# Kernel optimization log

Measured on AMD Instinct MI355X. Metric: run time of the kernel, lower is better.

## Reference

```python
import jax, jax.numpy as jnp
import numpy as np

B, N, H, NH, P = 32, 400, 512, 8, 3
DK = H // NH
SCALE = DK ** -0.5
EPS = 1e-5


def _ln(x, g, b):
    m = jnp.mean(x, axis=-1, keepdims=True)
    v = jnp.mean((x - m) ** 2, axis=-1, keepdims=True)
    return (x - m) * jax.lax.rsqrt(v + EPS) * g + b


def _split(x):  # [B,N,H] -> [B,h,N,dk]
    return x.reshape(x.shape[0], x.shape[1], NH, DK).transpose(0, 2, 1, 3)


def _merge(x):  # [B,h,N,dk] -> [B,N,H]
    return x.transpose(0, 2, 1, 3).reshape(x.shape[0], x.shape[2], H)


def _attn(q, k, v, mask):
    s = jnp.einsum('bhid,bhjd->bhij', q, k) * SCALE
    s = s * (1.0 + mask[:, None])  # learned multiplicative prior mask
    p = jax.nn.softmax(s, axis=-1)
    return jnp.einsum('bhij,bhjd->bhid', p, v)


def _weight_gen(pri, z, C, wq, keys, wf, bf):
    # pooled token query attends over the num_priors prior matrices
    qv = jnp.mean(z @ wq, axis=1)  # [B,H]
    aw = jax.nn.softmax((qv @ keys.T) * (H ** -0.5), axis=-1)  # [B,P]
    w = jnp.einsum('bp,bpij->bij', aw, pri)  # [B,N,N] fused prior mask
    fused = jnp.einsum('bij,bjh->bih', C, z) @ wf + bf  # [B,N,H] neighborhood fusion
    return w, aw, fused


def _ffn(x, w1, b1, w2, b2):
    return jax.nn.gelu(x @ w1 + b1, approximate=False) @ w2 + b2


def _forward(x_FC, x_SC, pri_FC, pri_SC, FC, SC, dw,
             ln_attn_FC_g, ln_attn_FC_b, ln_attn_SC_g, ln_attn_SC_b,
             ln_ffn_FC_g, ln_ffn_FC_b, ln_ffn_SC_g, ln_ffn_SC_b,
             qkv_FC_w, qkv_SC_w,
             ffn_FC_w1, ffn_FC_b1, ffn_FC_w2, ffn_FC_b2,
             ffn_SC_w1, ffn_SC_b1, ffn_SC_w2, ffn_SC_b2,
             wg_q_w, wg_keys, wg_fuse_w, wg_fuse_b,
             dist_in_FC_w, dist_in_FC_b, dist_in_SC_w, dist_in_SC_b,
             dist_out_FC_w, dist_out_FC_b, dist_out_SC_w, dist_out_SC_b):
    z_FC = _ln(x_FC, ln_attn_FC_g, ln_attn_FC_b)
    z_SC = _ln(x_SC, ln_attn_SC_g, ln_attn_SC_b)
    q_FC, k_FC, v_FC = [_split(t) for t in jnp.split(z_FC @ qkv_FC_w, 3, axis=-1)]
    q_SC, k_SC, v_SC = [_split(t) for t in jnp.split(z_SC @ qkv_SC_w, 3, axis=-1)]
    w_FC, aw_FC, fused_FC = _weight_gen(pri_FC, z_FC, FC, wg_q_w, wg_keys, wg_fuse_w, wg_fuse_b)
    w_SC, aw_SC, fused_SC = _weight_gen(pri_SC, z_SC, SC, wg_q_w, wg_keys, wg_fuse_w, wg_fuse_b)
    ctx_FC = _merge(_attn(q_FC, k_FC, v_FC, w_FC))
    ctx_SC = _merge(_attn(q_SC, k_SC, v_SC, w_SC))
    attn_out_FC = x_FC + ctx_FC + fused_FC
    attn_out_SC = x_SC + ctx_SC + fused_SC
    x_FC_new = attn_out_FC + _ffn(_ln(attn_out_FC, ln_ffn_FC_g, ln_ffn_FC_b), ffn_FC_w1, ffn_FC_b1, ffn_FC_w2, ffn_FC_b2)
    x_SC_new = attn_out_SC + _ffn(_ln(attn_out_SC, ln_ffn_SC_g, ln_ffn_SC_b), ffn_SC_w1, ffn_SC_b1, ffn_SC_w2, ffn_SC_b2)
    wf, ws = dw[0], dw[1]
    proj_FC = x_FC_new @ dist_in_FC_w + dist_in_FC_b
    proj_SC = x_SC_new @ dist_in_SC_w + dist_in_SC_b
    l_FC = jax.nn.log_softmax(proj_FC.reshape(-1, H), axis=-1)
    l_SC = jax.nn.log_softmax(proj_SC.reshape(-1, H), axis=-1)
    p_FC = jnp.exp(l_FC)
    p_SC = jnp.exp(l_SC)
    rows = jnp.float32(l_FC.shape[0])
    kl_FC = jnp.sum(p_SC * (l_SC - l_FC)) / rows  # KLDiv(batchmean)(l_FC, p_SC)
    kl_SC = jnp.sum(p_FC * (l_FC - l_SC)) / rows
    x_FC_out = (1.0 - wf) * x_FC_new + wf * (proj_FC @ dist_out_FC_w + dist_out_FC_b)
    x_SC_out = (1.0 - ws) * x_SC_new + ws * (proj_SC @ dist_out_SC_w + dist_out_SC_b)
    distill_loss = 0.5 * (kl_FC * wf + kl_SC * ws)
    return (x_FC_out, x_SC_out, distill_loss, aw_FC, aw_SC)


def setup_inputs() -> dict:
    key = jax.random.key(0)
    ks = jax.random.split(key, 24)
    init = lambda k, shape: 0.02 * jax.random.normal(k, shape, jnp.float32)
    d = {}
    d['x_FC'] = jax.random.normal(ks[0], (B, N, H), jnp.float32)
    d['x_SC'] = jax.random.normal(ks[1], (B, N, H), jnp.float32)
    d['pri_FC'] = jax.random.uniform(ks[2], (B, P, N, N), jnp.float32)
    d['pri_SC'] = jax.random.uniform(ks[3], (B, P, N, N), jnp.float32)
    d['FC'] = jax.random.uniform(ks[4], (B, N, N), jnp.float32)
    d['SC'] = jax.random.uniform(ks[5], (B, N, N), jnp.float32)
    d['dw'] = jnp.array([0.5, 0.5], jnp.float32)
    for nm in ['ln_attn_FC', 'ln_attn_SC', 'ln_ffn_FC', 'ln_ffn_SC']:
        d[nm + '_g'] = jnp.ones((H,), jnp.float32)
        d[nm + '_b'] = jnp.zeros((H,), jnp.float32)
    d['qkv_FC_w'] = init(ks[6], (H, 3 * H))
    d['qkv_SC_w'] = init(ks[7], (H, 3 * H))
    d['ffn_FC_w1'] = init(ks[8], (H, 4 * H)); d['ffn_FC_b1'] = jnp.zeros((4 * H,), jnp.float32)
    d['ffn_FC_w2'] = init(ks[9], (4 * H, H)); d['ffn_FC_b2'] = jnp.zeros((H,), jnp.float32)
    d['ffn_SC_w1'] = init(ks[10], (H, 4 * H)); d['ffn_SC_b1'] = jnp.zeros((4 * H,), jnp.float32)
    d['ffn_SC_w2'] = init(ks[11], (4 * H, H)); d['ffn_SC_b2'] = jnp.zeros((H,), jnp.float32)
    d['wg_q_w'] = init(ks[12], (H, H))
    d['wg_keys'] = init(ks[13], (P, H))
    d['wg_fuse_w'] = init(ks[14], (H, H)); d['wg_fuse_b'] = jnp.zeros((H,), jnp.float32)
    d['dist_in_FC_w'] = init(ks[15], (H, H)); d['dist_in_FC_b'] = jnp.zeros((H,), jnp.float32)
    d['dist_in_SC_w'] = init(ks[16], (H, H)); d['dist_in_SC_b'] = jnp.zeros((H,), jnp.float32)
    d['dist_out_FC_w'] = init(ks[17], (H, H)); d['dist_out_FC_b'] = jnp.zeros((H,), jnp.float32)
    d['dist_out_SC_w'] = init(ks[18], (H, H)); d['dist_out_SC_b'] = jnp.zeros((H,), jnp.float32)
    return d


def reference(x_FC, x_SC, pri_FC, pri_SC, FC, SC, dw,
              ln_attn_FC_g, ln_attn_FC_b, ln_attn_SC_g, ln_attn_SC_b,
              ln_ffn_FC_g, ln_ffn_FC_b, ln_ffn_SC_g, ln_ffn_SC_b,
              qkv_FC_w, qkv_SC_w,
              ffn_FC_w1, ffn_FC_b1, ffn_FC_w2, ffn_FC_b2,
              ffn_SC_w1, ffn_SC_b1, ffn_SC_w2, ffn_SC_b2,
              wg_q_w, wg_keys, wg_fuse_w, wg_fuse_b,
              dist_in_FC_w, dist_in_FC_b, dist_in_SC_w, dist_in_SC_b,
              dist_out_FC_w, dist_out_FC_b, dist_out_SC_w, dist_out_SC_b):
    return _forward(x_FC, x_SC, pri_FC, pri_SC, FC, SC, dw,
                    ln_attn_FC_g, ln_attn_FC_b, ln_attn_SC_g, ln_attn_SC_b,
                    ln_ffn_FC_g, ln_ffn_FC_b, ln_ffn_SC_g, ln_ffn_SC_b,
                    qkv_FC_w, qkv_SC_w,
                    ffn_FC_w1, ffn_FC_b1, ffn_FC_w2, ffn_FC_b2,
                    ffn_SC_w1, ffn_SC_b1, ffn_SC_w2, ffn_SC_b2,
                    wg_q_w, wg_keys, wg_fuse_w, wg_fuse_b,
                    dist_in_FC_w, dist_in_FC_b, dist_in_SC_w, dist_in_SC_b,
                    dist_out_FC_w, dist_out_FC_b, dist_out_SC_w, dist_out_SC_b)
```

## Files before the change

kernel.cpp:

```cpp
#include <hip/hip_runtime.h>
#include <hip/hip_bf16.h>
#include <math.h>

typedef __hip_bfloat16 bf16;

#define B_  32
#define N_  400
#define H_  512
#define NH_ 8
#define DK_ 64
#define P_  3
#define BN_ (B_*N_)
#define H3_ 1536
#define H4_ 2048

#define GLD16(g, l) __builtin_amdgcn_global_load_lds( \
    (__attribute__((address_space(1))) void*)(g), \
    (__attribute__((address_space(3))) void*)(l), 16, 0, 0)

__device__ __forceinline__ float b2f(bf16 v){ return __bfloat162float(v); }
__device__ __forceinline__ bf16  f2b(float v){ return __float2bfloat16(v); }
__device__ __forceinline__ float bfu(unsigned short u){ return __uint_as_float(((unsigned int)u)<<16); }
__device__ __forceinline__ unsigned short f2bu(float v){
  union { bf16 b; unsigned short u; } cv; cv.b = __float2bfloat16(v); return cv.u;
}
__device__ __forceinline__ bool is_f32(const void* gref){
  return *(const unsigned int*)gref == 0x3F800000u;
}
__device__ __forceinline__ float ldRaw(const void* p, long i, bool f32){
  return f32 ? ((const float*)p)[i] : b2f(((const bf16*)p)[i]);
}
__device__ __forceinline__ void stRaw(void* p, long i, float v, bool f32){
  if (f32) ((float*)p)[i] = v; else ((bf16*)p)[i] = f2b(v);
}

__device__ __forceinline__ float waveSum(float v){
  #pragma unroll
  for (int o=32;o>0;o>>=1) v += __shfl_xor(v,o,64);
  return v;
}
__device__ __forceinline__ float waveMax(float v){
  #pragma unroll
  for (int o=32;o>0;o>>=1) v = fmaxf(v,__shfl_xor(v,o,64));
  return v;
}
__device__ __forceinline__ float blockSum(float v, float* wred){
  v = waveSum(v);
  int w = threadIdx.x>>6, l = threadIdx.x&63;
  if (l==0) wred[w]=v;
  __syncthreads();
  float r = wred[0]+wred[1]+wred[2]+wred[3];
  __syncthreads();
  return r;
}
__device__ __forceinline__ float blockMax(float v, float* wred){
  v = waveMax(v);
  int w = threadIdx.x>>6, l = threadIdx.x&63;
  if (l==0) wred[w]=v;
  __syncthreads();
  float r = fmaxf(fmaxf(wred[0],wred[1]),fmaxf(wred[2],wred[3]));
  __syncthreads();
  return r;
}

template<int XMODE>
__global__ __launch_bounds__(256)
void ln_kernel(const void* __restrict__ x, const void* __restrict__ g,
               const void* __restrict__ bb, bf16* __restrict__ out,
               const void* __restrict__ gref)
{
  __shared__ float wred[4];
  const bool F32 = is_f32(gref);
  long row = blockIdx.x;
  int t = threadIdx.x;
  long base = row*H_;
  float v0, v1;
  if (XMODE==0){ v0 = ldRaw(x, base+t, F32); v1 = ldRaw(x, base+t+256, F32); }
  else         { v0 = b2f(((const bf16*)x)[base+t]); v1 = b2f(((const bf16*)x)[base+t+256]); }
  float mean = blockSum(v0+v1, wred) * (1.f/512.f);
  float d0 = v0-mean, d1 = v1-mean;
  float var = blockSum(d0*d0+d1*d1, wred) * (1.f/512.f);
  float rs = rsqrtf(var + 1e-5f);
  bf16* orow = out + base;
  orow[t]     = f2b(d0*rs*ldRaw(g,t,F32)     + ldRaw(bb,t,F32));
  orow[t+256] = f2b(d1*rs*ldRaw(g,t+256,F32) + ldRaw(bb,t+256,F32));
}

struct TC6 {
  const float* W[6];
  bf16* WT[6];
  int K[6]; int N[6]; int base[6];
};
__global__ __launch_bounds__(256)
void tc6_kernel(TC6 p)
{
  __shared__ float tile[32][33];
  int gt = blockIdx.x;
  int seg = 0;
  #pragma unroll
  for (int i=1;i<6;++i) if (gt >= p.base[i]) seg = i;
  int lt = gt - p.base[seg];
  int K = p.K[seg], N = p.N[seg];
  int ntx = N >> 5;
  int n0 = (lt % ntx)*32, k0 = (lt / ntx)*32;
  const float* W = p.W[seg];
  bf16* WT = p.WT[seg];
  int t = threadIdx.x;
  int c = t & 31, r = t >> 5;
  #pragma unroll
  for (int q=0;q<4;++q){
    int k = r + q*8;
    tile[k][c] = W[(long)(k0+k)*N + n0 + c];
  }
  __syncthreads();
  #pragma unroll
  for (int q=0;q<4;++q){
    int nn = r + q*8;
    WT[(long)(n0+nn)*K + k0 + c] = f2b(tile[c][nn]);
  }
}

__global__ __launch_bounds__(256)
void ztrans_kernel(const bf16* __restrict__ ZB, bf16* __restrict__ ZBT)
{
  __shared__ unsigned short tile[32][33];
  int j0 = blockIdx.x*32, h0 = blockIdx.y*32, b = blockIdx.z;
  int t = threadIdx.x;
  int c = t & 31, r = t >> 5;
  const unsigned short* src = (const unsigned short*)(ZB + (long)b*N_*H_);
  #pragma unroll
  for (int p=0;p<4;++p){
    int j = j0 + r + p*8;
    unsigned short v = 0;
    if (j < 400) v = src[(long)j*H_ + h0 + c];
    tile[r+p*8][c] = v;
  }
  __syncthreads();
  unsigned short* dst = (unsigned short*)(ZBT + (long)b*512*416);
  #pragma unroll
  for (int p=0;p<4;++p){
    int hh = r + p*8;
    dst[(long)(h0+hh)*416 + j0 + c] = tile[c][hh];
  }
}

__global__ __launch_bounds__(256)
void cconv_kernel(const float* __restrict__ C, bf16* __restrict__ CB)
{
  long u = ((long)blockIdx.x*256 + threadIdx.x)*8;
  int b = (int)(u / (512*416));
  int rem = (int)(u - (long)b*(512*416));
  int r = rem / 416, c = rem % 416;
  ushort4 lo = {0,0,0,0}, hi = {0,0,0,0};
  if (r < 400 && c < 400){
    const float* p = C + (long)b*160000 + r*400 + c;
    float4 f0 = *(const float4*)p;
    float4 f1 = *(const float4*)(p+4);
    lo.x=f2bu(f0.x); lo.y=f2bu(f0.y); lo.z=f2bu(f0.z); lo.w=f2bu(f0.w);
    hi.x=f2bu(f1.x); hi.y=f2bu(f1.y); hi.z=f2bu(f1.z); hi.w=f2bu(f1.w);
  }
  *(ushort4*)((unsigned short*)CB + u)     = lo;
  *(ushort4*)((unsigned short*)CB + u + 4) = hi;
}

__global__ __launch_bounds__(256)
void vtrans_kernel(const bf16* __restrict__ qkv, bf16* __restrict__ vtg)
{
  __shared__ unsigned short tile[32][33];
  int j0 = blockIdx.x*32, d0 = blockIdx.y*32, bh = blockIdx.z;
  int b = bh >> 3, h = bh & 7;
  int t = threadIdx.x;
  int c = t & 31, r = t >> 5;
  const unsigned short* src = (const unsigned short*)(qkv + (long)b*N_*H3_ + 1024 + h*64 + d0);
  #pragma unroll
  for (int p=0;p<4;++p){
    int j = j0 + r + p*8;
    unsigned short v = 0;
    if (j < 400) v = src[(long)j*H3_ + c];
    tile[r+p*8][c] = v;
  }
  __syncthreads();
  unsigned short* dst = (unsigned short*)(vtg + (long)bh*64*416);
  #pragma unroll
  for (int p=0;p<4;++p){
    int dd = r + p*8;
    dst[(long)(d0+dd)*416 + j0 + c] = tile[c][dd];
  }
}

template<int MI,int ACT,int RES,int OMODE>
__global__ __launch_bounds__(256)
void mgemm_kernel(const bf16* __restrict__ A, const bf16* __restrict__ BT,
                  const float* __restrict__ bias, const bf16* __restrict__ res,
                  void* __restrict__ out, long oOff,
                  int M, int K, int Nn,
                  long sA, long sW, long sO,
                  const float* __restrict__ dwp, int dwidx)
{
  typedef __attribute__((ext_vector_type(8))) short bf16x8;
  typedef __attribute__((ext_vector_type(4))) float f32x4;
  constexpr int BM = MI*32;
  constexpr int LPT = MI/2 + 2;
  __shared__ unsigned short As[3][BM*32];
  __shared__ unsigned short Bs[3][128*32];
  int t = threadIdx.x;
  int w = t >> 6, l = t & 63;
  int wm = (w >> 1)*(MI*16), wn = (w & 1)*64;
  int m0 = blockIdx.y*BM, n0 = blockIdx.x*128;
  long zA = (long)blockIdx.z*sA;
  const bf16* Ab = A + zA;
  const bf16* Bb = BT + (long)blockIdx.z*sW;
  long zO = (long)blockIdx.z*sO;
  f32x4 acc[MI][4] = {};
  int lrow = l & 15, lkc = l >> 4;
  int srow = t >> 2, skc = t & 3;
  int sk = (skc ^ ((srow >> 1) & 3))*8;
  int ck = (lkc ^ ((lrow >> 1) & 3))*8;
  int nk = K >> 5;

  auto STAGE = [&](int tile, int bufi){
    int kk = tile << 5;
    #pragma unroll
    for (int half=0; half<MI/2; ++half){
      const unsigned short* gA = (const unsigned short*)Ab + (long)(m0+srow+half*64)*K + kk + sk;
      GLD16(gA, &As[bufi][w*512 + half*2048]);
    }
    #pragma unroll
    for (int half=0; half<2; ++half){
      const unsigned short* gB = (const unsigned short*)Bb + (long)(n0+srow+half*64)*K + kk + sk;
      GLD16(gB, &Bs[bufi][w*512 + half*2048]);
    }
  };

  STAGE(0, 0);
  if (nk > 1) STAGE(1, 1);
  for (int kt=0; kt<nk; ++kt){
    int cur = kt % 3;
    if (kt+2 < nk) STAGE(kt+2, (kt+2)%3);
    if (kt+2 < nk)      asm volatile("s_waitcnt vmcnt(%0)" :: "i"(2*LPT) : "memory");
    else if (kt+1 < nk) asm volatile("s_waitcnt vmcnt(%0)" :: "i"(LPT)   : "memory");
    else                asm volatile("s_waitcnt vmcnt(0)" ::: "memory");
    __builtin_amdgcn_s_barrier();
    asm volatile("" ::: "memory");
    bf16x8 af[MI], bf_[4];
    #pragma unroll
    for (int i=0;i<MI;++i) af[i]  = *(const bf16x8*)&As[cur][(wm + i*16 + lrow)*32 + ck];
    #pragma unroll
    for (int i=0;i<4;++i)  bf_[i] = *(const bf16x8*)&Bs[cur][(wn + i*16 + lrow)*32 + ck];
    __builtin_amdgcn_s_setprio(1);
    #pragma unroll
    for (int mi=0;mi<MI;++mi)
      #pragma unroll
      for (int ni=0;ni<4;++ni)
        acc[mi][ni] = __builtin_amdgcn_mfma_f32_16x16x32_bf16(bf_[ni], af[mi], acc[mi][ni], 0, 0, 0);
    __builtin_amdgcn_s_setprio(0);
    asm volatile("" ::: "memory");
    __builtin_amdgcn_s_barrier();
  }
  float wbl = (RES==2) ? dwp[dwidx] : 0.f;
  #pragma unroll
  for (int mi=0;mi<MI;++mi){
    int gm = m0 + wm + mi*16 + lrow;
    if (gm >= M) continue;
    #pragma unroll
    for (int ni=0;ni<4;++ni){
      int gnb = n0 + wn + ni*16 + lkc*4;
      long o = zO + (long)gm*Nn + gnb;
      float v0 = acc[mi][ni][0], v1 = acc[mi][ni][1], v2 = acc[mi][ni][2], v3 = acc[mi][ni][3];
      if (bias){
        float4 bv = *(const float4*)&bias[gnb];
        v0 += bv.x; v1 += bv.y; v2 += bv.z; v3 += bv.w;
      }
      if (ACT==1){
        v0 = 0.5f*v0*(1.f + erff(v0*0.70710678118654752f));
        v1 = 0.5f*v1*(1.f + erff(v1*0.70710678118654752f));
        v2 = 0.5f*v2*(1.f + erff(v2*0.70710678118654752f));
        v3 = 0.5f*v3*(1.f + erff(v3*0.70710678118654752f));
      }
      if (RES==1){
        ushort4 r4 = *(const ushort4*)((const unsigned short*)res + o);
        v0 += bfu(r4.x); v1 += bfu(r4.y); v2 += bfu(r4.z); v3 += bfu(r4.w);
      }
      if (RES==2){
        ushort4 r4 = *(const ushort4*)((const unsigned short*)res + o);
        v0 = (1.f-wbl)*bfu(r4.x) + wbl*v0;
        v1 = (1.f-wbl)*bfu(r4.y) + wbl*v1;
        v2 = (1.f-wbl)*bfu(r4.z) + wbl*v2;
        v3 = (1.f-wbl)*bfu(r4.w) + wbl*v3;
      }
      if (OMODE==0){
        ushort4 o4;
        o4.x = f2bu(v0); o4.y = f2bu(v1); o4.z = f2bu(v2); o4.w = f2bu(v3);
        *(ushort4*)((unsigned short*)out + o) = o4;
      } else {
        *(float4*)((float*)out + oOff + o) = make_float4(v0,v1,v2,v3);
      }
    }
  }
}

__global__ __launch_bounds__(256)
void zbar_kernel(const bf16* __restrict__ Z, float* __restrict__ zbar)
{
  __shared__ float red[256];
  int hc = blockIdx.x, b = blockIdx.y;
  int t = threadIdx.x;
  int col = hc*64 + (t & 63), ns = t >> 6;
  const bf16* p = Z + (long)b*N_*H_ + (long)ns*100*H_ + col;
  float s = 0.f;
  for (int n=0;n<100;++n) s += b2f(p[(long)n*H_]);
  red[t] = s;
  __syncthreads();
  if (t < 64){
    float tot = red[t]+red[t+64]+red[t+128]+red[t+192];
    zbar[b*512 + hc*64 + t] = tot * (1.f/400.f);
  }
}

__global__ __launch_bounds__(256)
void qv_kernel(const float* __restrict__ zbar, const void* __restrict__ wq,
               float* __restrict__ qv, const void* __restrict__ gref)
{
  __shared__ float red[256];
  const bool F32 = is_f32(gref);
  int ch = blockIdx.x, b = blockIdx.y;
  int t = threadIdx.x;
  int col = ch*32 + (t & 31), ks = t >> 5;
  const float* zb = zbar + b*512;
  float s = 0.f;
  int k0 = ks*64;
  for (int k=0;k<64;++k)
    s = fmaf(zb[k0+k], ldRaw(wq, (long)(k0+k)*512 + col, F32), s);
  red[t] = s;
  __syncthreads();
  if (t < 32){
    float q = 0.f;
    #pragma unroll
    for (int i=0;i<8;++i) q += red[t + i*32];
    qv[b*512 + ch*32 + t] = q;
  }
}

__global__ __launch_bounds__(256)
void aw_kernel(const float* __restrict__ qv, const void* __restrict__ keys,
               float* __restrict__ awf, void* __restrict__ outbase, long offAw,
               const void* __restrict__ gref)
{
  __shared__ float wred[4];
  const bool F32 = is_f32(gref);
  int b = blockIdx.x, t = threadIdx.x;
  const float* q = qv + b*512;
  float lg[3];
  #pragma unroll
  for (int p=0;p<3;++p){
    float part = q[t]*ldRaw(keys, p*512+t, F32) + q[t+256]*ldRaw(keys, p*512+t+256, F32);
    lg[p] = blockSum(part, wred) * 0.04419417382415922f;
  }
  float m = fmaxf(lg[0], fmaxf(lg[1], lg[2]));
  float e0 = expf(lg[0]-m), e1 = expf(lg[1]-m), e2 = expf(lg[2]-m);
  float inv = 1.f/(e0+e1+e2);
  if (t<3){
    float a = (t==0?e0:(t==1?e1:e2))*inv;
    awf[b*3+t] = a;
    stRaw(outbase, offAw + b*3 + t, a, F32);
  }
}

__global__ __launch_bounds__(256)
void wcomb_kernel(const void* __restrict__ pri, const float* __restrict__ awf,
                  bf16* __restrict__ WM, const void* __restrict__ gref)
{
  const bool F32 = is_f32(gref);
  long u = (long)blockIdx.x*256 + threadIdx.x;
  long e0 = u*4;
  int b = (int)(e0 / 160000);
  long r = e0 - (long)b*160000;
  float a0 = awf[b*3+0], a1 = awf[b*3+1], a2 = awf[b*3+2];
  float o0,o1,o2,o3;
  if (F32){
    const float* p0 = (const float*)pri + (long)b*3*160000 + r;
    float4 a = *(const float4*)(p0);
    float4 c = *(const float4*)(p0 + 160000);
    float4 d = *(const float4*)(p0 + 320000);
    o0 = a0*a.x + a1*c.x + a2*d.x;
    o1 = a0*a.y + a1*c.y + a2*d.y;
    o2 = a0*a.z + a1*c.z + a2*d.z;
    o3 = a0*a.w + a1*c.w + a2*d.w;
  } else {
    const bf16* p0 = (const bf16*)pri + (long)b*3*160000 + r;
    ushort4 a = *(const ushort4*)(p0);
    ushort4 c = *(const ushort4*)(p0 + 160000);
    ushort4 d = *(const ushort4*)(p0 + 320000);
    o0 = a0*bfu(a.x) + a1*bfu(c.x) + a2*bfu(d.x);
    o1 = a0*bfu(a.y) + a1*bfu(c.y) + a2*bfu(d.y);
    o2 = a0*bfu(a.z) + a1*bfu(c.z) + a2*bfu(d.z);
    o3 = a0*bfu(a.w) + a1*bfu(c.w) + a2*bfu(d.w);
  }
  ushort4 o;
  o.x = f2bu(o0); o.y = f2bu(o1); o.z = f2bu(o2); o.w = f2bu(o3);
  *(ushort4*)(WM + e0) = o;
}

__global__ __launch_bounds__(128)
void attn_kernel(const bf16* __restrict__ qkv, const bf16* __restrict__ wm,
                 const bf16* __restrict__ vtg, const void* __restrict__ x,
                 const bf16* __restrict__ fused, bf16* __restrict__ aout,
                 const void* __restrict__ gref)
{
  typedef __attribute__((ext_vector_type(8))) short bf16x8;
  typedef __attribute__((ext_vector_type(4))) float f32x4;
  __shared__ unsigned short Pbuf[2][2][16*40];
  const bool F32 = is_f32(gref);
  int t = threadIdx.x, wv = t >> 6, l = t & 63;
  int h = blockIdx.x, b = blockIdx.y;
  int qt = blockIdx.z*2 + wv;
  if (qt >= 25) return;
  int lr = l & 15, lg = l >> 4;
  int i0 = qt*16;
  const bf16* qb = qkv + (long)b*N_*H3_ + h*64;
  const bf16* kb = qb + 512;
  const bf16* wrow = wm + (long)b*N_*N_;
  const bf16* vt = vtg + (long)(b*NH_ + h)*64*416;
  bf16x8 qf0 = *(const bf16x8*)(qb + (long)(i0+lr)*H3_ + lg*8);
  bf16x8 qf1 = *(const bf16x8*)(qb + (long)(i0+lr)*H3_ + 32 + lg*8);
  float rm = -1e30f, rl = 0.f;
  f32x4 o[4] = {};
  #pragma unroll
  for (int w=0; w<13; ++w){
    int t0 = 2*w, t1 = 2*w+1;
    f32x4 s0, s1;
    {
      bf16x8 kf0 = *(const bf16x8*)(kb + (long)(t0*16+lr)*H3_ + lg*8);
      bf16x8 kf1 = *(const bf16x8*)(kb + (long)(t0*16+lr)*H3_ + 32 + lg*8);
      f32x4 st = {0.f,0.f,0.f,0.f};
      st = __builtin_amdgcn_mfma_f32_16x16x32_bf16(kf0, qf0, st, 0,0,0);
      st = __builtin_amdgcn_mfma_f32_16x16x32_bf16(kf1, qf1, st, 0,0,0);
      uint2 w4 = *(const uint2*)(wrow + (long)(i0+lr)*400 + t0*16 + lg*4);
      s0[0] = st[0]*0.125f*(1.f + bfu((unsigned short)(w4.x & 0xffffu)));
      s0[1] = st[1]*0.125f*(1.f + bfu((unsigned short)(w4.x >> 16)));
      s0[2] = st[2]*0.125f*(1.f + bfu((unsigned short)(w4.y & 0xffffu)));
      s0[3] = st[3]*0.125f*(1.f + bfu((unsigned short)(w4.y >> 16)));
    }
    if (t1 < 25){
      bf16x8 kf0 = *(const bf16x8*)(kb + (long)(t1*16+lr)*H3_ + lg*8);
      bf16x8 kf1 = *(const bf16x8*)(kb + (long)(t1*16+lr)*H3_ + 32 + lg*8);
      f32x4 st = {0.f,0.f,0.f,0.f};
      st = __builtin_amdgcn_mfma_f32_16x16x32_bf16(kf0, qf0, st, 0,0,0);
      st = __builtin_amdgcn_mfma_f32_16x16x32_bf16(kf1, qf1, st, 0,0,0);
      uint2 w4 = *(const uint2*)(wrow + (long)(i0+lr)*400 + t1*16 + lg*4);
      s1[0] = st[0]*0.125f*(1.f + bfu((unsigned short)(w4.x & 0xffffu)));
      s1[1] = st[1]*0.125f*(1.f + bfu((unsigned short)(w4.x >> 16)));
      s1[2] = st[2]*0.125f*(1.f + bfu((unsigned short)(w4.y & 0xffffu)));
      s1[3] = st[3]*0.125f*(1.f + bfu((unsigned short)(w4.y >> 16)));
    } else {
      s1[0]=s1[1]=s1[2]=s1[3] = -1e30f;
    }
    float tm = fmaxf(fmaxf(fmaxf(s0[0],s0[1]), fmaxf(s0[2],s0[3])),
                     fmaxf(fmaxf(s1[0],s1[1]), fmaxf(s1[2],s1[3])));
    tm = fmaxf(tm, __shfl_xor(tm, 16));
    tm = fmaxf(tm, __shfl_xor(tm, 32));
    float mn = fmaxf(rm, tm);
    float sc = __expf(rm - mn);
    unsigned pk0x, pk0y, pk1x = 0u, pk1y = 0u;
    float ls = 0.f;
    {
      unsigned u0 = f2bu(__expf(s0[0]-mn)), u1 = f2bu(__expf(s0[1]-mn));
      unsigned u2 = f2bu(__expf(s0[2]-mn)), u3 = f2bu(__expf(s0[3]-mn));
      pk0x = u0 | (u1<<16); pk0y = u2 | (u3<<16);
      ls += __uint_as_float(u0<<16) + __uint_as_float(u1<<16)
          + __uint_as_float(u2<<16) + __uint_as_float(u3<<16);
    }
    if (t1 < 25){
      unsigned u0 = f2bu(__expf(s1[0]-mn)), u1 = f2bu(__expf(s1[1]-mn));
      unsigned u2 = f2bu(__expf(s1[2]-mn)), u3 = f2bu(__expf(s1[3]-mn));
      pk1x = u0 | (u1<<16); pk1y = u2 | (u3<<16);
      ls += __uint_as_float(u0<<16) + __uint_as_float(u1<<16)
          + __uint_as_float(u2<<16) + __uint_as_float(u3<<16);
    }
    ls += __shfl_xor(ls, 16);
    ls += __shfl_xor(ls, 32);
    rl = rl*sc + ls;
    rm = mn;
    unsigned short* pb = Pbuf[wv][w & 1];
    *(uint2*)&pb[lr*40 + lg*4]      = make_uint2(pk0x, pk0y);
    *(uint2*)&pb[lr*40 + 16 + lg*4] = make_uint2(pk1x, pk1y);
    bf16x8 pa = *(const bf16x8*)&pb[lr*40 + lg*8];
    float sq0 = __shfl(sc, lg*4 + 0);
    float sq1 = __shfl(sc, lg*4 + 1);
    float sq2 = __shfl(sc, lg*4 + 2);
    float sq3 = __shfl(sc, lg*4 + 3);
    #pragma unroll
    for (int dt=0; dt<4; ++dt){
      o[dt][0] *= sq0; o[dt][1] *= sq1; o[dt][2] *= sq2; o[dt][3] *= sq3;
      bf16x8 vf = *(const bf16x8*)(vt + (long)(dt*16+lr)*416 + w*32 + lg*8);
      o[dt] = __builtin_amdgcn_mfma_f32_16x16x32_bf16(pa, vf, o[dt], 0,0,0);
    }
  }
  float invl = 1.f/rl;
  #pragma unroll
  for (int q=0;q<4;++q){
    float iv = __shfl(invl, lg*4 + q);
    long gi = (long)(b*N_ + i0 + lg*4 + q);
    #pragma unroll
    for (int dt=0;dt<4;++dt){
      long oi = gi*H_ + h*64 + dt*16 + lr;
      float xv = F32 ? ((const float*)x)[oi] : b2f(((const bf16*)x)[oi]);
      float fv = b2f(fused[oi]);
      aout[oi] = f2b(o[dt][q]*iv + xv + fv);
    }
  }
}

__global__ __launch_bounds__(256)
void kl_rows_kernel(const bf16* __restrict__ pF, const bf16* __restrict__ pS,
                    float2* __restrict__ rowpart)
{
  __shared__ float wred[4];
  long row = blockIdx.x;
  int t = threadIdx.x;
  const bf16* fr = pF + row*512;
  const bf16* sr = pS + row*512;
  float f0 = b2f(fr[t]), f1 = b2f(fr[t+256]), s0 = b2f(sr[t]), s1 = b2f(sr[t+256]);
  float mF = blockMax(fmaxf(f0,f1), wred);
  float mS = blockMax(fmaxf(s0,s1), wred);
  float sumF = blockSum(__expf(f0-mF)+__expf(f1-mF), wred);
  float sumS = blockSum(__expf(s0-mS)+__expf(s1-mS), wred);
  float lseF = mF + __logf(sumF), lseS = mS + __logf(sumS);
  float lF0 = f0-lseF, lF1 = f1-lseF, lS0 = s0-lseS, lS1 = s1-lseS;
  float pS0 = __expf(lS0), pS1 = __expf(lS1), pF0 = __expf(lF0), pF1 = __expf(lF1);
  float a  = pS0*(lS0-lF0) + pS1*(lS1-lF1);
  float bb = pF0*(lF0-lS0) + pF1*(lF1-lS1);
  a  = blockSum(a,  wred);
  bb = blockSum(bb, wred);
  if (t==0) rowpart[row] = make_float2(a, bb);
}

__global__ __launch_bounds__(256)
void kl_final_kernel(const float2* __restrict__ rowpart, const void* __restrict__ dw,
                     void* __restrict__ outbase, long offLoss,
                     const void* __restrict__ gref)
{
  __shared__ float wred[4];
  const bool F32 = is_f32(gref);
  int t = threadIdx.x;
  float sa=0.f, sb=0.f;
  for (int i=t;i<BN_;i+=256){ float2 v = rowpart[i]; sa+=v.x; sb+=v.y; }
  sa = blockSum(sa, wred);
  sb = blockSum(sb, wred);
  if (t==0){
    float wf = ldRaw(dw,0,F32), ws = ldRaw(dw,1,F32);
    float loss = 0.5f*((sa/12800.f)*wf + (sb/12800.f)*ws);
    stRaw(outbase, offLoss, loss, F32);
  }
}

#define OFF_ZB    0L
#define OFF_QKV   13107200L
#define OFF_FUSED 52428800L
#define OFF_WM    65536000L
#define OFF_CZ    75776000L
#define OFF_PROJ0 88883200L
#define OFF_PROJ1 101990400L
#define OFF_QKVT  115097600L
#define OFF_W1T   116670464L
#define OFF_W2T   118767616L
#define OFF_FUT   120864768L
#define OFF_DIT   121389056L
#define OFF_DOT   121913344L
#define OFF_ZBT   122437632L
#define OFF_ZBAR  136069120L
#define OFF_AWF   136134656L
#define OFF_ROWP  136135680L
#define OFF_VTG   136238080L
#define OFF_QV    149869568L

extern "C" void kernel_launch(void* const* d_in, const int* in_sizes, int n_in,
                              void* d_out, int out_size, void* d_ws, size_t ws_size,
                              hipStream_t stream)
{
  (void)in_sizes; (void)n_in; (void)out_size; (void)ws_size;
  const void* x[2]    = {d_in[0],  d_in[1]};
  const void* pri[2]  = {d_in[2],  d_in[3]};
  const float* Cm[2]  = {(const float*)d_in[4], (const float*)d_in[5]};
  const float* dwf    =  (const float*)d_in[6];
  const void* lnag[2] = {d_in[7],  d_in[9]};
  const void* lnab[2] = {d_in[8],  d_in[10]};
  const void* lnfg[2] = {d_in[11], d_in[13]};
  const void* lnfb[2] = {d_in[12], d_in[14]};
  const float* qkvw[2]= {(const float*)d_in[15], (const float*)d_in[16]};
  const float* fw1[2] = {(const float*)d_in[17], (const float*)d_in[21]};
  const float* fb1[2] = {(const float*)d_in[18], (const float*)d_in[22]};
  const float* fw2[2] = {(const float*)d_in[19], (const float*)d_in[23]};
  const float* fb2[2] = {(const float*)d_in[20], (const float*)d_in[24]};
  const void* wgq     =  d_in[25];
  const void* wgk     =  d_in[26];
  const float* wgfw   =  (const float*)d_in[27];
  const float* wgfb   =  (const float*)d_in[28];
  const float* diw[2] = {(const float*)d_in[29], (const float*)d_in[31]};
  const float* dib[2] = {(const float*)d_in[30], (const float*)d_in[32]};
  const float* dow[2] = {(const float*)d_in[33], (const float*)d_in[35]};
  const float* dob[2] = {(const float*)d_in[34], (const float*)d_in[36]};
  const void* gref    =  d_in[7];

  char* ws = (char*)d_ws;
  bf16*  ZB    = (bf16*)(ws + OFF_ZB);
  bf16*  LN2   = (bf16*)(ws + OFF_ZB);
  bf16*  XNEW  = (bf16*)(ws + OFF_ZB);
  bf16*  QKV   = (bf16*)(ws + OFF_QKV);
  bf16*  HH    = (bf16*)(ws + OFF_QKV);
  bf16*  FUSED = (bf16*)(ws + OFF_FUSED);
  bf16*  WM    = (bf16*)(ws + OFF_WM);
  bf16*  CZ    = (bf16*)(ws + OFF_CZ);
  bf16*  AOUT  = (bf16*)(ws + OFF_CZ);
  bf16*  PROJ[2] = {(bf16*)(ws + OFF_PROJ0), (bf16*)(ws + OFF_PROJ1)};
  bf16*  QKVT  = (bf16*)(ws + OFF_QKVT);
  bf16*  W1T   = (bf16*)(ws + OFF_W1T);
  bf16*  W2T   = (bf16*)(ws + OFF_W2T);
  bf16*  FUT   = (bf16*)(ws + OFF_FUT);
  bf16*  DIT   = (bf16*)(ws + OFF_DIT);
  bf16*  DOT   = (bf16*)(ws + OFF_DOT);
  bf16*  ZBT   = (bf16*)(ws + OFF_ZBT);
  bf16*  VTG   = (bf16*)(ws + OFF_VTG);
  bf16*  CB    = (bf16*)(ws + OFF_VTG);
  float* ZBAR  = (float*)(ws + OFF_ZBAR);
  float* AWF   = (float*)(ws + OFF_AWF);
  float2* ROWP = (float2*)(ws + OFF_ROWP);
  float* QV    = (float*)(ws + OFF_QV);

  const long offX[2]  = {0L, 6553600L};
  const long offLoss  = 13107200L;
  const long offAw[2] = {13107201L, 13107297L};

  for (int s=0; s<2; ++s){
    TC6 tp;
    tp.W[0]=qkvw[s]; tp.WT[0]=QKVT; tp.K[0]=512;  tp.N[0]=1536;
    tp.W[1]=fw1[s];  tp.WT[1]=W1T;  tp.K[1]=512;  tp.N[1]=2048;
    tp.W[2]=fw2[s];  tp.WT[2]=W2T;  tp.K[2]=2048; tp.N[2]=512;
    tp.W[3]=wgfw;    tp.WT[3]=FUT;  tp.K[3]=512;  tp.N[3]=512;
    tp.W[4]=diw[s];  tp.WT[4]=DIT;  tp.K[4]=512;  tp.N[4]=512;
    tp.W[5]=dow[s];  tp.WT[5]=DOT;  tp.K[5]=512;  tp.N[5]=512;
    tp.base[0]=0; tp.base[1]=768; tp.base[2]=1792; tp.base[3]=2816;
    tp.base[4]=3072; tp.base[5]=3328;
    tc6_kernel<<<3584,256,0,stream>>>(tp);
    ln_kernel<0><<<BN_,256,0,stream>>>(x[s], lnag[s], lnab[s], ZB, gref);
    zbar_kernel<<<dim3(8,B_),256,0,stream>>>(ZB, ZBAR);
    ztrans_kernel<<<dim3(13,16,32),256,0,stream>>>(ZB, ZBT);
    cconv_kernel<<<3328,256,0,stream>>>(Cm[s], CB);
    mgemm_kernel<4,0,0,0><<<dim3(12,100,1),256,0,stream>>>(
        ZB, QKVT, nullptr, nullptr, QKV, 0, BN_, 512, H3_, 0,0,0, nullptr,0);
    qv_kernel<<<dim3(16,B_),256,0,stream>>>(ZBAR, wgq, QV, gref);
    aw_kernel<<<B_,256,0,stream>>>(QV, wgk, AWF, d_out, offAw[s], gref);
    wcomb_kernel<<<5000,256,0,stream>>>(pri[s], AWF, WM, gref);
    mgemm_kernel<4,0,0,0><<<dim3(4,4,32),256,0,stream>>>(
        CB, ZBT, nullptr, nullptr, CZ, 0, 400, 416, 512,
        212992L, 212992L, 204800L, nullptr,0);
    mgemm_kernel<2,0,0,0><<<dim3(4,200,1),256,0,stream>>>(
        CZ, FUT, wgfb, nullptr, FUSED, 0, BN_, 512, 512, 0,0,0, nullptr,0);
    vtrans_kernel<<<dim3(13,2,256),256,0,stream>>>(QKV, VTG);
    attn_kernel<<<dim3(NH_,B_,13),128,0,stream>>>(QKV, WM, VTG, x[s], FUSED, AOUT, gref);
    ln_kernel<1><<<BN_,256,0,stream>>>(AOUT, lnfg[s], lnfb[s], LN2, gref);
    mgemm_kernel<4,1,0,0><<<dim3(16,100,1),256,0,stream>>>(
        LN2, W1T, fb1[s], nullptr, HH, 0, BN_, 512, H4_, 0,0,0, nullptr,0);
    mgemm_kernel<2,0,1,0><<<dim3(4,200,1),256,0,stream>>>(
        HH, W2T, fb2[s], AOUT, XNEW, 0, BN_, 2048, 512, 0,0,0, nullptr,0);
    mgemm_kernel<2,0,0,0><<<dim3(4,200,1),256,0,stream>>>(
        XNEW, DIT, dib[s], nullptr, PROJ[s], 0, BN_, 512, 512, 0,0,0, nullptr,0);
    mgemm_kernel<2,0,2,1><<<dim3(4,200,1),256,0,stream>>>(
        PROJ[s], DOT, dob[s], XNEW, d_out, offX[s], BN_, 512, 512, 0,0,0, dwf, s);
  }
  kl_rows_kernel<<<BN_,256,0,stream>>>(PROJ[0], PROJ[1], ROWP);
  kl_final_kernel<<<1,256,0,stream>>>(ROWP, dwf, d_out, offLoss, gref);
}
```

Before: 920.5 us.

## Switch GEMM to 64-wide K tiles with double buffering

The MFMA GEMM kernel now stages 64-element K slices with a two-buffer pipeline instead of 32-element slices with three buffers. This halves the number of barrier and wait iterations and issues two MFMA passes per stage, using an XOR swizzle widened to eight chunks. Because K must now be a multiple of 64, the padded inner dimension for the C·z batched GEMM grows from 416 to 448, and the transpose and convert kernels and workspace offsets are resized to match. The risk is less prefetch depth and more LDS per block, which may lower occupancy.

```diff
diff --git a/kernel.cpp b/kernel.cpp
--- a/kernel.cpp
+++ b/kernel.cpp
@@ -13,6 +13,7 @@
 #define BN_ (B_*N_)
 #define H3_ 1536
 #define H4_ 2048
+#define KP_ 448
 
 #define GLD16(g, l) __builtin_amdgcn_global_load_lds( \
     (__attribute__((address_space(1))) void*)(g), \
@@ -136,11 +137,11 @@
     tile[r+p*8][c] = v;
   }
   __syncthreads();
-  unsigned short* dst = (unsigned short*)(ZBT + (long)b*512*416);
+  unsigned short* dst = (unsigned short*)(ZBT + (long)b*512*KP_);
   #pragma unroll
   for (int p=0;p<4;++p){
     int hh = r + p*8;
-    dst[(long)(h0+hh)*416 + j0 + c] = tile[c][hh];
+    dst[(long)(h0+hh)*KP_ + j0 + c] = tile[c][hh];
   }
 }
 
@@ -148,9 +149,9 @@
 void cconv_kernel(const float* __restrict__ C, bf16* __restrict__ CB)
 {
   long u = ((long)blockIdx.x*256 + threadIdx.x)*8;
-  int b = (int)(u / (512*416));
-  int rem = (int)(u - (long)b*(512*416));
-  int r = rem / 416, c = rem % 416;
+  int b = (int)(u / (512*KP_));
+  int rem = (int)(u - (long)b*(512*KP_));
+  int r = rem / KP_, c = rem % KP_;
   ushort4 lo = {0,0,0,0}, hi = {0,0,0,0};
   if (r < 400 && c < 400){
     const float* p = C + (long)b*160000 + r*400 + c;
@@ -200,62 +201,72 @@
   typedef __attribute__((ext_vector_type(8))) short bf16x8;
   typedef __attribute__((ext_vector_type(4))) float f32x4;
   constexpr int BM = MI*32;
-  constexpr int LPT = MI/2 + 2;
-  __shared__ unsigned short As[3][BM*32];
-  __shared__ unsigned short Bs[3][128*32];
+  constexpr int LPT = MI + 4;
+  __shared__ unsigned short As[2][BM*64];
+  __shared__ unsigned short Bs[2][128*64];
   int t = threadIdx.x;
   int w = t >> 6, l = t & 63;
   int wm = (w >> 1)*(MI*16), wn = (w & 1)*64;
   int m0 = blockIdx.y*BM, n0 = blockIdx.x*128;
-  long zA = (long)blockIdx.z*sA;
-  const bf16* Ab = A + zA;
+  const bf16* Ab = A + (long)blockIdx.z*sA;
   const bf16* Bb = BT + (long)blockIdx.z*sW;
   long zO = (long)blockIdx.z*sO;
   f32x4 acc[MI][4] = {};
   int lrow = l & 15, lkc = l >> 4;
-  int srow = t >> 2, skc = t & 3;
-  int sk = (skc ^ ((srow >> 1) & 3))*8;
-  int ck = (lkc ^ ((lrow >> 1) & 3))*8;
-  int nk = K >> 5;
+  int srow = t >> 3, skc = t & 7;
+  int sk = (skc ^ (srow & 7))*8;
+  int c0 = ((0*4 + lkc) ^ (lrow & 7))*8;
+  int c1 = ((1*4 + lkc) ^ (lrow & 7))*8;
+  int nk = K >> 6;
+  int buf = 0;
 
   auto STAGE = [&](int tile, int bufi){
-    int kk = tile << 5;
-    #pragma unroll
-    for (int half=0; half<MI/2; ++half){
-      const unsigned short* gA = (const unsigned short*)Ab + (long)(m0+srow+half*64)*K + kk + sk;
-      GLD16(gA, &As[bufi][w*512 + half*2048]);
-    }
-    #pragma unroll
-    for (int half=0; half<2; ++half){
-      const unsigned short* gB = (const unsigned short*)Bb + (long)(n0+srow+half*64)*K + kk + sk;
-      GLD16(gB, &Bs[bufi][w*512 + half*2048]);
+    int kk = tile << 6;
+    #pragma unroll
+    for (int r=0; r<MI; ++r){
+      const unsigned short* gA = (const unsigned short*)Ab + (long)(m0+srow+r*32)*K + kk + sk;
+      GLD16(gA, &As[bufi][t*8 + r*2048]);
+    }
+    #pragma unroll
+    for (int r=0; r<4; ++r){
+      const unsigned short* gB = (const unsigned short*)Bb + (long)(n0+srow+r*32)*K + kk + sk;
+      GLD16(gB, &Bs[bufi][t*8 + r*2048]);
     }
   };
 
   STAGE(0, 0);
-  if (nk > 1) STAGE(1, 1);
   for (int kt=0; kt<nk; ++kt){
-    int cur = kt % 3;
-    if (kt+2 < nk) STAGE(kt+2, (kt+2)%3);
-    if (kt+2 < nk)      asm volatile("s_waitcnt vmcnt(%0)" :: "i"(2*LPT) : "memory");
-    else if (kt+1 < nk) asm volatile("s_waitcnt vmcnt(%0)" :: "i"(LPT)   : "memory");
-    else                asm volatile("s_waitcnt vmcnt(0)" ::: "memory");
+    if (kt+1 < nk) STAGE(kt+1, buf^1);
+    if (kt+1 < nk) asm volatile("s_waitcnt vmcnt(%0)" :: "i"(LPT) : "memory");
+    else           asm volatile("s_waitcnt vmcnt(0)" ::: "memory");
     __builtin_amdgcn_s_barrier();
     asm volatile("" ::: "memory");
-    bf16x8 af[MI], bf_[4];
-    #pragma unroll
-    for (int i=0;i<MI;++i) af[i]  = *(const bf16x8*)&As[cur][(wm + i*16 + lrow)*32 + ck];
-    #pragma unroll
-    for (int i=0;i<4;++i)  bf_[i] = *(const bf16x8*)&Bs[cur][(wn + i*16 + lrow)*32 + ck];
+    bf16x8 af0[MI], af1[MI], bf0[4], bf1[4];
+    #pragma unroll
+    for (int i=0;i<MI;++i){
+      af0[i] = *(const bf16x8*)&As[buf][(wm + i*16 + lrow)*64 + c0];
+      af1[i] = *(const bf16x8*)&As[buf][(wm + i*16 + lrow)*64 + c1];
+    }
+    #pragma unroll
+    for (int i=0;i<4;++i){
+      bf0[i] = *(const bf16x8*)&Bs[buf][(wn + i*16 + lrow)*64 + c0];
+      bf1[i] = *(const bf16x8*)&Bs[buf][(wn + i*16 + lrow)*64 + c1];
+    }
     __builtin_amdgcn_s_setprio(1);
     #pragma unroll
     for (int mi=0;mi<MI;++mi)
       #pragma unroll
       for (int ni=0;ni<4;++ni)
-        acc[mi][ni] = __builtin_amdgcn_mfma_f32_16x16x32_bf16(bf_[ni], af[mi], acc[mi][ni], 0, 0, 0);
+        acc[mi][ni] = __builtin_amdgcn_mfma_f32_16x16x32_bf16(bf0[ni], af0[mi], acc[mi][ni], 0, 0, 0);
+    #pragma unroll
+    for (int mi=0;mi<MI;++mi)
+      #pragma unroll
+      for (int ni=0;ni<4;++ni)
+        acc[mi][ni] = __builtin_amdgcn_mfma_f32_16x16x32_bf16(bf1[ni], af1[mi], acc[mi][ni], 0, 0, 0);
     __builtin_amdgcn_s_setprio(0);
     asm volatile("" ::: "memory");
     __builtin_amdgcn_s_barrier();
+    buf ^= 1;
   }
   float wbl = (RES==2) ? dwp[dwidx] : 0.f;
   #pragma unroll
@@ -568,11 +579,11 @@
 #define OFF_DIT   121389056L
 #define OFF_DOT   121913344L
 #define OFF_ZBT   122437632L
-#define OFF_ZBAR  136069120L
-#define OFF_AWF   136134656L
-#define OFF_ROWP  136135680L
-#define OFF_VTG   136238080L
-#define OFF_QV    149869568L
+#define OFF_ZBAR  137117696L
+#define OFF_AWF   137183232L
+#define OFF_ROWP  137184256L
+#define OFF_VTG   137286656L
+#define OFF_QV    151966720L
 
 extern "C" void kernel_launch(void* const* d_in, const int* in_sizes, int n_in,
                               void* d_out, int out_size, void* d_ws, size_t ws_size,
@@ -644,16 +655,16 @@
     tc6_kernel<<<3584,256,0,stream>>>(tp);
     ln_kernel<0><<<BN_,256,0,stream>>>(x[s], lnag[s], lnab[s], ZB, gref);
     zbar_kernel<<<dim3(8,B_),256,0,stream>>>(ZB, ZBAR);
-    ztrans_kernel<<<dim3(13,16,32),256,0,stream>>>(ZB, ZBT);
-    cconv_kernel<<<3328,256,0,stream>>>(Cm[s], CB);
+    ztrans_kernel<<<dim3(14,16,32),256,0,stream>>>(ZB, ZBT);
+    cconv_kernel<<<3584,256,0,stream>>>(Cm[s], CB);
     mgemm_kernel<4,0,0,0><<<dim3(12,100,1),256,0,stream>>>(
         ZB, QKVT, nullptr, nullptr, QKV, 0, BN_, 512, H3_, 0,0,0, nullptr,0);
     qv_kernel<<<dim3(16,B_),256,0,stream>>>(ZBAR, wgq, QV, gref);
     aw_kernel<<<B_,256,0,stream>>>(QV, wgk, AWF, d_out, offAw[s], gref);
     wcomb_kernel<<<5000,256,0,stream>>>(pri[s], AWF, WM, gref);
     mgemm_kernel<4,0,0,0><<<dim3(4,4,32),256,0,stream>>>(
-        CB, ZBT, nullptr, nullptr, CZ, 0, 400, 416, 512,
-        212992L, 212992L, 204800L, nullptr,0);
+        CB, ZBT, nullptr, nullptr, CZ, 0, 400, KP_, 512,
+        (long)512*KP_, (long)512*KP_, 204800L, nullptr,0);
     mgemm_kernel<2,0,0,0><<<dim3(4,200,1),256,0,stream>>>(
         CZ, FUT, wgfb, nullptr, FUSED, 0, BN_, 512, 512, 0,0,0, nullptr,0);
     vtrans_kernel<<<dim3(13,2,256),256,0,stream>>>(QKV, VTG);
```

Measured after the change: 971.9 us. +5.6%, slower.
